# Kernel tuning notes

Hardware: AMD Instinct MI355X
Metric: run time of the kernel (lower is better)

The kernel has to match this reference:

```python
import jax, jax.numpy as jnp
from jax import lax
import numpy as np

K = 256   # kernel_size == hidden channels (Haar basis size)
S = 16    # stride
BN_EPS = 1e-5


def _haar_matrix_unnorm(n):
    if n == 2:
        return np.array([[1.0, 1.0], [1.0, -1.0]])
    prev = _haar_matrix_unnorm(n // 2)
    top = np.kron(prev, np.array([1.0, 1.0]))
    bot = np.kron(np.eye(n // 2), np.array([1.0, -1.0]))
    return np.concatenate((top, bot))


def haar_matrix(n):
    h = _haar_matrix_unnorm(n)
    return h / np.linalg.norm(h, axis=1, keepdims=True)


def setup_inputs() -> dict:
    key = jax.random.key(0)
    ks = jax.random.split(key, 8)
    B, T = 64, 32768
    haar = jnp.asarray(haar_matrix(K), dtype=jnp.float32)          # [K, K]
    x = jax.random.normal(ks[0], (B, 1, T), dtype=jnp.float32)
    return {
        "x": x,
        # BitwiseConv1d(1, K, K, stride=S, padding=K)
        "conv_w": haar[:, None, :],                                 # [K, 1, K] (OIH)
        "conv_b": 0.01 * jax.random.normal(ks[1], (K,), dtype=jnp.float32),
        "conv_gate": jax.random.uniform(ks[2], (K, 1, K), dtype=jnp.float32),
        "conv_scale": jnp.ones((K,), dtype=jnp.float32),            # adaptive per-out-channel scale
        # BatchNorm1d(K)
        "bn_gamma": jnp.ones((K,), dtype=jnp.float32),
        "bn_beta": jnp.zeros((K,), dtype=jnp.float32),
        # BitwiseConvTranspose1d(K, 1, K, stride=S)
        "ct_w": haar.T[:, None, :],                                 # [K(in), 1(out), K] (IOH, torch layout)
        "ct_b": 0.01 * jax.random.normal(ks[3], (1,), dtype=jnp.float32),
        "ct_gate": jax.random.uniform(ks[4], (K, 1, K), dtype=jnp.float32),
        "ct_scale": jnp.ones((1,), dtype=jnp.float32),
    }


def _forward(x, conv_w, conv_b, conv_gate, conv_scale, bn_gamma, bn_beta,
             ct_w, ct_b, ct_gate, ct_scale):
    T = x.shape[2]
    # --- BitwiseConv1d: gated weights (in_bin/weight_bin = identity) ---
    # gate binarization maps gate -> (gate + 1) / 2, multiplied into weights
    w = conv_w * (conv_gate + 1.0) * 0.5                            # [K,1,K]
    h = lax.conv_general_dilated(
        x, w, window_strides=(S,), padding=[(K, K)],
        dimension_numbers=("NCH", "OIH", "NCH"))                  # [B,K,L]
    h = conv_scale[None, :, None] * (h + conv_b[None, :, None])    # adaptive scaling
    # --- ReLU then BatchNorm1d (training-mode batch statistics) ---
    h = jax.nn.relu(h)
    mu = jnp.mean(h, axis=(0, 2), keepdims=True)
    var = jnp.mean((h - mu) ** 2, axis=(0, 2), keepdims=True)
    h = (h - mu) * lax.rsqrt(var + BN_EPS)
    h = h * bn_gamma[None, :, None] + bn_beta[None, :, None]
    # --- BitwiseConvTranspose1d: gated weights, expressed as dilated conv ---
    wt = ct_w * (ct_gate + 1.0) * 0.5                               # [K_in, 1, K]
    # torch IOH -> regular-conv OIH with kernel flipped
    wr = jnp.flip(jnp.transpose(wt, (1, 0, 2)), axis=-1)            # [1, K, K]
    y = lax.conv_general_dilated(
        h, wr, window_strides=(1,), padding=[(K - 1, K - 1)],
        lhs_dilation=(S,), dimension_numbers=("NCH", "OIH", "NCH"))
    y = ct_scale[None, :, None] * (y + ct_b[None, :, None])
    # crop: out[:, :, K : T + K]
    return y[:, :, K:T + K]


def reference(x, conv_w, conv_b, conv_gate, conv_scale, bn_gamma, bn_beta,
              ct_w, ct_b, ct_gate, ct_scale):
    return _forward(x, conv_w, conv_b, conv_gate, conv_scale, bn_gamma, bn_beta,
                    ct_w, ct_b, ct_gate, ct_scale)
```

## Files before the change

kernel.cpp:

```cpp
#include <hip/hip_runtime.h>
#include <hip/hip_bf16.h>

#define BB 64
#define TT 32768
#define KK 256
#define LL 2065
#define NLT 9
#define NPART (BB*NLT)
#define NJ 19
#define HBSTR 72
#define NPT3 8

typedef __attribute__((ext_vector_type(8))) short short8;
typedef __attribute__((ext_vector_type(4))) float f32x4;
typedef __attribute__((ext_vector_type(4))) int int4v;
typedef __attribute__((ext_vector_type(2))) unsigned int uint2v;

__device__ __forceinline__ unsigned short f2bf(float f) {
    unsigned u = __builtin_bit_cast(unsigned, f);
    unsigned r = (u + 0x7FFFu + ((u >> 16) & 1u)) >> 16;
    return (unsigned short)r;
}
__device__ __forceinline__ unsigned pkbf(float a, float b) {
    unsigned r;
    asm("v_cvt_pk_bf16_f32 %0, %1, %2" : "=v"(r) : "v"(a), "v"(b));
    return r;
}
__device__ __forceinline__ void gload_lds16(const void* g, void* l) {
    __builtin_amdgcn_global_load_lds(
        (const __attribute__((address_space(1))) unsigned int*)g,
        (__attribute__((address_space(3))) unsigned int*)l, 16, 0, 0);
}

__global__ void k0_w1f(const float* __restrict__ cw, const float* __restrict__ cgt,
                       unsigned short* __restrict__ W1f)
{
    int idx = blockIdx.x*256 + threadIdx.x;
    int lane = idx & 63, ntL = (idx>>6)&7, kk = (idx>>9)&7, half = idx>>12;
    int o = half*128 + ntL*16 + (lane&15);
    int kbase = kk*32 + ((lane>>4)<<3);
    short8 v;
    #pragma unroll
    for (int i = 0; i < 8; ++i) {
        int gi = o*KK + kbase + i;
        v[i] = (short)f2bf(cw[gi]*(cgt[gi]+1.0f)*0.5f);
    }
    *(short8*)(W1f + (size_t)idx*8) = v;
}

__global__ __launch_bounds__(256, 3)
void k1_conv(const float* __restrict__ x, const float* __restrict__ cs,
             const float* __restrict__ cb, const unsigned short* __restrict__ W1f,
             unsigned short* __restrict__ hout,
             float* __restrict__ psum, float* __restrict__ psq)
{
    __shared__ __align__(16) char smem[13056 + 32768];
    char* xwinb = smem;
    char* wbuf  = smem + 13056;
    unsigned short* hb = (unsigned short*)smem;
    float* redS = (float*)(smem + 36864);
    float* redQ = (float*)(smem + 36864 + 1024);

    const int tid   = threadIdx.x;
    const int q     = blockIdx.x & 3;
    const int ltile = blockIdx.x >> 2;
    const int b     = blockIdx.y;
    const int l0    = ltile * 256;
    const long pos0 = (long)l0*16 - 256;
    const int lane  = tid & 63;
    const int w     = tid >> 6;

    {
        #pragma unroll
        for (int it = 0; it < 8; ++it) {
            int ci = w*8 + it;
            int kk = ci >> 2, ntl = ci & 3;
            size_t so = (size_t)((((q>>1)*8 + kk)*8 + (q&1)*4 + ntl))*1024;
            gload_lds16((const char*)W1f + so + lane*16, wbuf + ci*1024);
        }
    }
    {
        const float* xs = x + (size_t)b*TT;
        for (int g = tid; g < 272; g += 256) {
            long base = pos0 + (long)g*16;
            unsigned uu[8];
            if (base >= 0 && base + 16 <= (long)TT) {
                const float4* xv = (const float4*)(xs + base);
                float4 a0 = xv[0], a1 = xv[1], a2 = xv[2], a3 = xv[3];
                uu[0] = pkbf(a0.x, a0.y); uu[1] = pkbf(a0.z, a0.w);
                uu[2] = pkbf(a1.x, a1.y); uu[3] = pkbf(a1.z, a1.w);
                uu[4] = pkbf(a2.x, a2.y); uu[5] = pkbf(a2.z, a2.w);
                uu[6] = pkbf(a3.x, a3.y); uu[7] = pkbf(a3.z, a3.w);
            } else {
                #pragma unroll
                for (int m = 0; m < 16; m += 2) {
                    long p = base + m;
                    float f0 = (p   >= 0 && p   < TT) ? xs[p]   : 0.0f;
                    float f1 = (p+1 >= 0 && p+1 < TT) ? xs[p+1] : 0.0f;
                    uu[m>>1] = pkbf(f0, f1);
                }
            }
            int4v w0 = { (int)uu[0], (int)uu[1], (int)uu[2], (int)uu[3] };
            int4v w1 = { (int)uu[4], (int)uu[5], (int)uu[6], (int)uu[7] };
            *(int4v*)(xwinb + 48*g)      = w0;
            *(int4v*)(xwinb + 48*g + 16) = w1;
        }
    }
    __syncthreads();

    f32x4 acc[4][4];
    #pragma unroll
    for (int mt = 0; mt < 4; ++mt)
        #pragma unroll
        for (int nt = 0; nt < 4; ++nt) acc[mt][nt] = (f32x4){0.f,0.f,0.f,0.f};

    const int gq = lane >> 4;
    const int Gt = 16*gq + 16*(gq>>1);
    const int abase = 48*((w<<6) + (lane & 15)) + Gt;

    #pragma unroll
    for (int kk = 0; kk < 8; ++kk) {
        short8 bfx[4], afw[4];
        #pragma unroll
        for (int nt = 0; nt < 4; ++nt)
            bfx[nt] = *(const short8*)(xwinb + abase + nt*768 + kk*96);
        #pragma unroll
        for (int mt = 0; mt < 4; ++mt)
            afw[mt] = *(const short8*)(wbuf + (kk*4 + mt)*1024 + lane*16);
        __builtin_amdgcn_s_setprio(1);
        #pragma unroll
        for (int mt = 0; mt < 4; ++mt)
            #pragma unroll
            for (int nt = 0; nt < 4; ++nt)
                acc[mt][nt] = __builtin_amdgcn_mfma_f32_16x16x32_bf16(afw[mt], bfx[nt], acc[mt][nt], 0, 0, 0);
        __builtin_amdgcn_s_setprio(0);
    }
    __syncthreads();

    const int c0 = q*64;
    const int g  = lane >> 4;
    const int li = lane & 15;
    #pragma unroll
    for (int mt = 0; mt < 4; ++mt) {
        int cq = c0 + mt*16 + g*4;
        f32x4 cs4 = *(const f32x4*)&cs[cq];
        f32x4 cb4 = *(const f32x4*)&cb[cq];
        f32x4 s4 = (f32x4){0.f,0.f,0.f,0.f};
        f32x4 q4 = (f32x4){0.f,0.f,0.f,0.f};
        #pragma unroll
        for (int nt = 0; nt < 4; ++nt) {
            int lloc = (w<<6) + nt*16 + li;
            f32x4 hv;
            #pragma unroll
            for (int rr = 0; rr < 4; ++rr)
                hv[rr] = fmaxf(cs4[rr]*(acc[mt][nt][rr] + cb4[rr]), 0.0f);
            uint2v pkv = { pkbf(hv[0], hv[1]), pkbf(hv[2], hv[3]) };
            *(uint2v*)(hb + lloc*HBSTR + mt*16 + g*4) = pkv;
            if (l0 + lloc < LL) { s4 += hv; q4 += hv*hv; }
        }
        #pragma unroll
        for (int d = 1; d < 16; d <<= 1) {
            #pragma unroll
            for (int rr = 0; rr < 4; ++rr) {
                s4[rr] += __shfl_xor(s4[rr], d);
                q4[rr] += __shfl_xor(q4[rr], d);
            }
        }
        if (li == 0) {
            *(f32x4*)&redS[((w*4 + mt)*4 + g)*4] = s4;
            *(f32x4*)&redQ[((w*4 + mt)*4 + g)*4] = q4;
        }
    }
    __syncthreads();

    {
        const int rsub = tid >> 3;
        const int cpos = tid & 7;
        #pragma unroll
        for (int it = 0; it < 8; ++it) {
            int row = it*32 + rsub;
            int l = l0 + row;
            if (l < LL) {
                int4v v = *(const int4v*)(hb + row*HBSTR + cpos*8);
                *(int4v*)(hout + (((size_t)(b*LL + l)) << 8) + q*64 + cpos*8) = v;
            }
        }
    }
    if (tid < 64) {
        int mt = tid >> 4, gg = (tid >> 2) & 3, rr = tid & 3;
        float s = 0.f, qq = 0.f;
        #pragma unroll
        for (int wv = 0; wv < 4; ++wv) {
            s  += redS[((wv*4 + mt)*4 + gg)*4 + rr];
            qq += redQ[((wv*4 + mt)*4 + gg)*4 + rr];
        }
        int c = c0 + tid;
        int slot = b*NLT + ltile;
        psum[c*NPART + slot] = s;
        psq [c*NPART + slot] = qq;
    }
}

__global__ __launch_bounds__(256)
void k2_bn(const float* __restrict__ psum, const float* __restrict__ psq,
           const float* __restrict__ bng, const float* __restrict__ bnb,
           const float* __restrict__ ctw, const float* __restrict__ ctg,
           const float* __restrict__ ctscale,
           float* __restrict__ W3s, float* __restrict__ SWS)
{
    __shared__ double rs[4], rq[4];
    __shared__ float s_a, s_bc;
    __shared__ float swl[256];
    const int c = blockIdx.x;
    const int tid = threadIdx.x;
    double s = 0.0, q = 0.0;
    for (int i = tid; i < NPART; i += 256) {
        s += (double)psum[c*NPART + i];
        q += (double)psq [c*NPART + i];
    }
    for (int off = 32; off > 0; off >>= 1) {
        s += __shfl_down(s, off);
        q += __shfl_down(q, off);
    }
    if ((tid & 63) == 0) { rs[tid >> 6] = s; rq[tid >> 6] = q; }
    __syncthreads();
    if (tid == 0) {
        double st = rs[0]+rs[1]+rs[2]+rs[3];
        double qt = rq[0]+rq[1]+rq[2]+rq[3];
        const double cnt = (double)BB * (double)LL;
        double mu = st / cnt;
        double var = qt / cnt - mu*mu;
        float rsig = (float)(1.0 / sqrt(var + 1e-5));
        float a = bng[c] * rsig;
        s_a = a;
        s_bc = bnb[c] - (float)mu * a;
    }
    __syncthreads();
    float a = s_a, bc = s_bc, scl = ctscale[0];
    int gi = c*KK + tid;
    float wt = ctw[gi] * (ctg[gi] + 1.0f) * 0.5f;
    W3s[tid*KK + c] = scl * a * wt;
    swl[tid] = wt * bc;
    __syncthreads();
    if (tid < 16) {
        float acc2 = 0.0f;
        #pragma unroll
        for (int d = 0; d < 16; ++d) acc2 += swl[d*16 + tid];
        SWS[c*16 + tid] = acc2;
    }
}

__global__ void k2b_const(const float* __restrict__ SWS, const float* __restrict__ ctb,
                          const float* __restrict__ ctscale, float* __restrict__ C2)
{
    int r = threadIdx.x;
    if (r < 16) {
        float s = 0.0f;
        for (int c = 0; c < 256; ++c) s += SWS[c*16 + r];
        C2[r] = ctscale[0] * (s + ctb[0]);
    }
}

__global__ void k2c_b2f(const float* __restrict__ W3s, unsigned short* __restrict__ B2f)
{
    int idx = blockIdx.x*256 + threadIdx.x;
    int lane = idx & 63;
    int ntG  = (idx>>6) & 3;
    int kk   = (idx>>8) & 7;
    int j    = idx>>11;
    int c    = kk*32 + ((lane>>4)<<3);
    int r    = lane & 15;
    int d    = ntG + 15 - j;
    short8 v;
    if (d >= 0 && d <= 15) {
        const float* wr = W3s + (size_t)(16*d + r)*KK + c;
        #pragma unroll
        for (int i = 0; i < 8; ++i) v[i] = (short)f2bf(wr[i]);
    } else {
        #pragma unroll
        for (int i = 0; i < 8; ++i) v[i] = 0;
    }
    *(short8*)(B2f + (size_t)idx*8) = v;
}

__global__ __launch_bounds__(512, 1)
void k3_synth(const unsigned short* __restrict__ h, const unsigned short* __restrict__ B2f,
              const float* __restrict__ C2, float* __restrict__ out)
{
    __shared__ __align__(16) char As[272*512];
    const int tid  = threadIdx.x;
    const int lane = tid & 63;
    const int w    = tid >> 6;
    const int b    = blockIdx.y;
    const int P0   = blockIdx.x * 64;

    const char* hbase = (const char*)h + (((size_t)(b*LL) + 4*P0 + 1) << 9);

    {
        const int rl = lane >> 5;
        #pragma unroll
        for (int i = 0; i < 17; ++i) {
            int r0  = w*34 + i*2;
            int row = r0 + rl;
            int chunk = (lane & 31) ^ ((row >> 2) & 7);
            gload_lds16(hbase + (size_t)row*512 + chunk*16, As + r0*512);
        }
    }
    __syncthreads();

    const int li = lane & 15;
    const int gq = lane >> 4;

    f32x4 acc[4][4];
    #pragma unroll
    for (int mt = 0; mt < 4; ++mt)
        #pragma unroll
        for (int nt = 0; nt < 4; ++nt) acc[mt][nt] = (f32x4){0.f,0.f,0.f,0.f};

    #pragma unroll 1
    for (int jj = 0; jj < 3; ++jj) {
        const int j = w + jj*8;
        if (j >= NJ) break;
        short8 bfA[4], bfB[4];
        #pragma unroll
        for (int nt = 0; nt < 4; ++nt)
            bfA[nt] = *(const short8*)(B2f + (((size_t)(j*8 + 0)*4 + nt)*64 + lane)*8);
        #pragma unroll
        for (int kk = 0; kk < 8; ++kk) {
            if (kk < 7) {
                #pragma unroll
                for (int nt = 0; nt < 4; ++nt)
                    bfB[nt] = *(const short8*)(B2f + (((size_t)(j*8 + kk+1)*4 + nt)*64 + lane)*8);
            }
            short8 af[4];
            #pragma unroll
            for (int mt = 0; mt < 4; ++mt) {
                int row = 64*mt + 4*li + j;
                int p = (kk*4 + gq) ^ ((row >> 2) & 7);
                af[mt] = *(const short8*)(As + row*512 + p*16);
            }
            __builtin_amdgcn_s_setprio(1);
            #pragma unroll
            for (int mt = 0; mt < 4; ++mt)
                #pragma unroll
                for (int nt = 0; nt < 4; ++nt)
                    acc[mt][nt] = __builtin_amdgcn_mfma_f32_16x16x32_bf16(af[mt], bfA[nt], acc[mt][nt], 0, 0, 0);
            __builtin_amdgcn_s_setprio(0);
            #pragma unroll
            for (int nt = 0; nt < 4; ++nt) bfA[nt] = bfB[nt];
        }
    }
    __syncthreads();

    float* red = (float*)As;
    #pragma unroll
    for (int mt = 0; mt < 4; ++mt)
        #pragma unroll
        for (int nt = 0; nt < 4; ++nt) {
            int u = nt*16 + li;
            #pragma unroll
            for (int rr = 0; rr < 4; ++rr) {
                int Pl = 16*mt + gq*4 + rr;
                red[w*4352 + Pl*68 + u] = acc[mt][nt][rr];
            }
        }
    __syncthreads();

    {
        float* ob = out + (size_t)b*TT + (size_t)P0*64;
        #pragma unroll
        for (int it = 0; it < 2; ++it) {
            int item = it*512 + tid;
            int P = item >> 4, uq = item & 15;
            f32x4 s = (f32x4){0.f,0.f,0.f,0.f};
            #pragma unroll
            for (int c = 0; c < 8; ++c)
                s += *(const f32x4*)&red[c*4352 + P*68 + uq*4];
            int ub = (uq & 3)*4;
            f32x4 c2v = { C2[ub], C2[ub+1], C2[ub+2], C2[ub+3] };
            *(f32x4*)&ob[P*64 + uq*4] = s + c2v;
        }
    }
}

extern "C" void kernel_launch(void* const* d_in, const int* in_sizes, int n_in,
                              void* d_out, int out_size, void* d_ws, size_t ws_size,
                              hipStream_t stream)
{
    const float* x       = (const float*)d_in[0];
    const float* cw      = (const float*)d_in[1];
    const float* cb      = (const float*)d_in[2];
    const float* cgt     = (const float*)d_in[3];
    const float* cs      = (const float*)d_in[4];
    const float* bng     = (const float*)d_in[5];
    const float* bnb     = (const float*)d_in[6];
    const float* ctw     = (const float*)d_in[7];
    const float* ctb     = (const float*)d_in[8];
    const float* ctg     = (const float*)d_in[9];
    const float* ctscale = (const float*)d_in[10];
    float* out = (float*)d_out;

    char* ws = (char*)d_ws;
    size_t off = 0;
    unsigned short* h    = (unsigned short*)(ws + off); off += (size_t)BB*LL*KK*2;
    float* psum          = (float*)(ws + off);          off += (size_t)KK*NPART*4;
    float* psq           = (float*)(ws + off);          off += (size_t)KK*NPART*4;
    unsigned short* W1f  = (unsigned short*)(ws + off); off += 65536*2;
    float* W3s           = (float*)(ws + off);          off += (size_t)KK*KK*4;
    float* SWS           = (float*)(ws + off);          off += (size_t)KK*16*4;
    float* C2            = (float*)(ws + off);          off += 64;
    unsigned short* B2f  = (unsigned short*)(ws + off); off += (size_t)NJ*8*4*64*8*2;

    k0_w1f  <<<32, 256, 0, stream>>>(cw, cgt, W1f);
    k1_conv <<<dim3(36, BB), 256, 0, stream>>>(x, cs, cb, W1f, h, psum, psq);
    k2_bn   <<<KK, 256, 0, stream>>>(psum, psq, bng, bnb, ctw, ctg, ctscale, W3s, SWS);
    k2b_const<<<1, 64, 0, stream>>>(SWS, ctb, ctscale, C2);
    k2c_b2f <<<152, 256, 0, stream>>>(W3s, B2f);
    k3_synth<<<dim3(NPT3, BB), 512, 0, stream>>>(h, B2f, C2, out);
}
```

Before: 83.52 us.

## Halve synthesis tile, fold conv scale into weights, shorten BN shuffle reduction

The synthesis kernel now processes 32 output frames per block instead of 64. That halves its LDS footprint and accumulator count, allows up to 4 blocks per CU, and doubles the grid. The conv scale is folded into the bf16 weights and a precomputed scaled bias, which removes a multiply per output in the conv epilogue. The per-channel stats reduction does fewer cross-lane shuffles and writes more partials to LDS, which are summed afterwards. Smaller tiles mean less reuse of each B2f fragment load, and folding the scale into the weights before bf16 rounding slightly changes numerics.

```diff
diff --git a/kernel.cpp b/kernel.cpp
--- a/kernel.cpp
+++ b/kernel.cpp
@@ -9,7 +9,7 @@
 #define NPART (BB*NLT)
 #define NJ 19
 #define HBSTR 72
-#define NPT3 8
+#define NPT3 16
 
 typedef __attribute__((ext_vector_type(8))) short short8;
 typedef __attribute__((ext_vector_type(4))) float f32x4;
@@ -33,24 +33,30 @@
 }
 
 __global__ void k0_w1f(const float* __restrict__ cw, const float* __restrict__ cgt,
-                       unsigned short* __restrict__ W1f)
+                       const float* __restrict__ cs, const float* __restrict__ cb,
+                       unsigned short* __restrict__ W1f, float* __restrict__ cbs)
 {
     int idx = blockIdx.x*256 + threadIdx.x;
     int lane = idx & 63, ntL = (idx>>6)&7, kk = (idx>>9)&7, half = idx>>12;
     int o = half*128 + ntL*16 + (lane&15);
+    float sc = cs[o];
     int kbase = kk*32 + ((lane>>4)<<3);
     short8 v;
     #pragma unroll
     for (int i = 0; i < 8; ++i) {
         int gi = o*KK + kbase + i;
-        v[i] = (short)f2bf(cw[gi]*(cgt[gi]+1.0f)*0.5f);
+        v[i] = (short)f2bf(sc * cw[gi]*(cgt[gi]+1.0f)*0.5f);
     }
     *(short8*)(W1f + (size_t)idx*8) = v;
+    if (blockIdx.x == 0) {
+        int c = threadIdx.x;
+        cbs[c] = cs[c]*cb[c];
+    }
 }
 
 __global__ __launch_bounds__(256, 3)
-void k1_conv(const float* __restrict__ x, const float* __restrict__ cs,
-             const float* __restrict__ cb, const unsigned short* __restrict__ W1f,
+void k1_conv(const float* __restrict__ x, const float* __restrict__ cbs,
+             const unsigned short* __restrict__ W1f,
              unsigned short* __restrict__ hout,
              float* __restrict__ psum, float* __restrict__ psq)
 {
@@ -59,7 +65,7 @@
     char* wbuf  = smem + 13056;
     unsigned short* hb = (unsigned short*)smem;
     float* redS = (float*)(smem + 36864);
-    float* redQ = (float*)(smem + 36864 + 1024);
+    float* redQ = (float*)(smem + 36864 + 4096);
 
     const int tid   = threadIdx.x;
     const int q     = blockIdx.x & 3;
@@ -143,8 +149,7 @@
     #pragma unroll
     for (int mt = 0; mt < 4; ++mt) {
         int cq = c0 + mt*16 + g*4;
-        f32x4 cs4 = *(const f32x4*)&cs[cq];
-        f32x4 cb4 = *(const f32x4*)&cb[cq];
+        f32x4 cbs4 = *(const f32x4*)&cbs[cq];
         f32x4 s4 = (f32x4){0.f,0.f,0.f,0.f};
         f32x4 q4 = (f32x4){0.f,0.f,0.f,0.f};
         #pragma unroll
@@ -153,22 +158,23 @@
             f32x4 hv;
             #pragma unroll
             for (int rr = 0; rr < 4; ++rr)
-                hv[rr] = fmaxf(cs4[rr]*(acc[mt][nt][rr] + cb4[rr]), 0.0f);
+                hv[rr] = fmaxf(acc[mt][nt][rr] + cbs4[rr], 0.0f);
             uint2v pkv = { pkbf(hv[0], hv[1]), pkbf(hv[2], hv[3]) };
             *(uint2v*)(hb + lloc*HBSTR + mt*16 + g*4) = pkv;
             if (l0 + lloc < LL) { s4 += hv; q4 += hv*hv; }
         }
         #pragma unroll
-        for (int d = 1; d < 16; d <<= 1) {
+        for (int d = 1; d < 4; d <<= 1) {
             #pragma unroll
             for (int rr = 0; rr < 4; ++rr) {
                 s4[rr] += __shfl_xor(s4[rr], d);
                 q4[rr] += __shfl_xor(q4[rr], d);
             }
         }
-        if (li == 0) {
-            *(f32x4*)&redS[((w*4 + mt)*4 + g)*4] = s4;
-            *(f32x4*)&redQ[((w*4 + mt)*4 + g)*4] = q4;
+        if ((li & 3) == 0) {
+            int slot = ((w*4 + mt)*4 + g)*4 + (li >> 2);
+            *(f32x4*)&redS[slot*4] = s4;
+            *(f32x4*)&redQ[slot*4] = q4;
         }
     }
     __syncthreads();
@@ -190,10 +196,13 @@
         int mt = tid >> 4, gg = (tid >> 2) & 3, rr = tid & 3;
         float s = 0.f, qq = 0.f;
         #pragma unroll
-        for (int wv = 0; wv < 4; ++wv) {
-            s  += redS[((wv*4 + mt)*4 + gg)*4 + rr];
-            qq += redQ[((wv*4 + mt)*4 + gg)*4 + rr];
-        }
+        for (int wv = 0; wv < 4; ++wv)
+            #pragma unroll
+            for (int l4 = 0; l4 < 4; ++l4) {
+                int slot = ((wv*4 + mt)*4 + gg)*4 + l4;
+                s  += redS[slot*4 + rr];
+                qq += redQ[slot*4 + rr];
+            }
         int c = c0 + tid;
         int slot = b*NLT + ltile;
         psum[c*NPART + slot] = s;
@@ -283,24 +292,24 @@
     *(short8*)(B2f + (size_t)idx*8) = v;
 }
 
-__global__ __launch_bounds__(512, 1)
+__global__ __launch_bounds__(512, 4)
 void k3_synth(const unsigned short* __restrict__ h, const unsigned short* __restrict__ B2f,
               const float* __restrict__ C2, float* __restrict__ out)
 {
-    __shared__ __align__(16) char As[272*512];
+    __shared__ __align__(16) char As[144*512];
     const int tid  = threadIdx.x;
     const int lane = tid & 63;
     const int w    = tid >> 6;
     const int b    = blockIdx.y;
-    const int P0   = blockIdx.x * 64;
+    const int P0   = blockIdx.x * 32;
 
     const char* hbase = (const char*)h + (((size_t)(b*LL) + 4*P0 + 1) << 9);
 
     {
         const int rl = lane >> 5;
         #pragma unroll
-        for (int i = 0; i < 17; ++i) {
-            int r0  = w*34 + i*2;
+        for (int i = 0; i < 9; ++i) {
+            int r0  = w*18 + i*2;
             int row = r0 + rl;
             int chunk = (lane & 31) ^ ((row >> 2) & 7);
             gload_lds16(hbase + (size_t)row*512 + chunk*16, As + r0*512);
@@ -311,9 +320,9 @@
     const int li = lane & 15;
     const int gq = lane >> 4;
 
-    f32x4 acc[4][4];
-    #pragma unroll
-    for (int mt = 0; mt < 4; ++mt)
+    f32x4 acc[2][4];
+    #pragma unroll
+    for (int mt = 0; mt < 2; ++mt)
         #pragma unroll
         for (int nt = 0; nt < 4; ++nt) acc[mt][nt] = (f32x4){0.f,0.f,0.f,0.f};
 
@@ -332,16 +341,16 @@
                 for (int nt = 0; nt < 4; ++nt)
                     bfB[nt] = *(const short8*)(B2f + (((size_t)(j*8 + kk+1)*4 + nt)*64 + lane)*8);
             }
-            short8 af[4];
-            #pragma unroll
-            for (int mt = 0; mt < 4; ++mt) {
+            short8 af[2];
+            #pragma unroll
+            for (int mt = 0; mt < 2; ++mt) {
                 int row = 64*mt + 4*li + j;
                 int p = (kk*4 + gq) ^ ((row >> 2) & 7);
                 af[mt] = *(const short8*)(As + row*512 + p*16);
             }
             __builtin_amdgcn_s_setprio(1);
             #pragma unroll
-            for (int mt = 0; mt < 4; ++mt)
+            for (int mt = 0; mt < 2; ++mt)
                 #pragma unroll
                 for (int nt = 0; nt < 4; ++nt)
                     acc[mt][nt] = __builtin_amdgcn_mfma_f32_16x16x32_bf16(af[mt], bfA[nt], acc[mt][nt], 0, 0, 0);
@@ -354,32 +363,28 @@
 
     float* red = (float*)As;
     #pragma unroll
-    for (int mt = 0; mt < 4; ++mt)
+    for (int mt = 0; mt < 2; ++mt)
         #pragma unroll
         for (int nt = 0; nt < 4; ++nt) {
             int u = nt*16 + li;
             #pragma unroll
             for (int rr = 0; rr < 4; ++rr) {
                 int Pl = 16*mt + gq*4 + rr;
-                red[w*4352 + Pl*68 + u] = acc[mt][nt][rr];
+                red[w*2176 + Pl*68 + u] = acc[mt][nt][rr];
             }
         }
     __syncthreads();
 
     {
+        int P = tid >> 4, uq = tid & 15;
+        f32x4 s = (f32x4){0.f,0.f,0.f,0.f};
+        #pragma unroll
+        for (int c = 0; c < 8; ++c)
+            s += *(const f32x4*)&red[c*2176 + P*68 + uq*4];
+        int ub = (uq & 3)*4;
+        f32x4 c2v = { C2[ub], C2[ub+1], C2[ub+2], C2[ub+3] };
         float* ob = out + (size_t)b*TT + (size_t)P0*64;
-        #pragma unroll
-        for (int it = 0; it < 2; ++it) {
-            int item = it*512 + tid;
-            int P = item >> 4, uq = item & 15;
-            f32x4 s = (f32x4){0.f,0.f,0.f,0.f};
-            #pragma unroll
-            for (int c = 0; c < 8; ++c)
-                s += *(const f32x4*)&red[c*4352 + P*68 + uq*4];
-            int ub = (uq & 3)*4;
-            f32x4 c2v = { C2[ub], C2[ub+1], C2[ub+2], C2[ub+3] };
-            *(f32x4*)&ob[P*64 + uq*4] = s + c2v;
-        }
+        *(f32x4*)&ob[P*64 + uq*4] = s + c2v;
     }
 }
 
@@ -409,10 +414,11 @@
     float* W3s           = (float*)(ws + off);          off += (size_t)KK*KK*4;
     float* SWS           = (float*)(ws + off);          off += (size_t)KK*16*4;
     float* C2            = (float*)(ws + off);          off += 64;
+    float* cbs           = (float*)(ws + off);          off += 1024;
     unsigned short* B2f  = (unsigned short*)(ws + off); off += (size_t)NJ*8*4*64*8*2;
 
-    k0_w1f  <<<32, 256, 0, stream>>>(cw, cgt, W1f);
-    k1_conv <<<dim3(36, BB), 256, 0, stream>>>(x, cs, cb, W1f, h, psum, psq);
+    k0_w1f  <<<32, 256, 0, stream>>>(cw, cgt, cs, cb, W1f, cbs);
+    k1_conv <<<dim3(36, BB), 256, 0, stream>>>(x, cbs, W1f, h, psum, psq);
     k2_bn   <<<KK, 256, 0, stream>>>(psum, psq, bng, bnb, ctw, ctg, ctscale, W3s, SWS);
     k2b_const<<<1, 64, 0, stream>>>(SWS, ctb, ctscale, C2);
     k2c_b2f <<<152, 256, 0, stream>>>(W3s, B2f);
```

Result: no change. 84.87 us (+1.6%).

## Split synthesis GEMM over K halves into two launches and skip zero weight tiles

Applied to the files above, without the earlier changes.

k3_synth now processes one half of the channel dimension per launch (z=0,1), using 256-thread blocks with half the LDS so two blocks fit per CU. The second launch reads back the first's partial output and adds the bias. Each wave gets a contiguous range of j values and skips MFMAs on B2f tiles that are known to be all zero. k2b_const's serial reduction becomes a 256-thread two-level reduction. The split adds an extra launch plus an output read-modify-write pass, and 19 j-values spread over 4 waves leaves them unevenly loaded.

```diff
diff --git a/kernel.cpp b/kernel.cpp
--- a/kernel.cpp
+++ b/kernel.cpp
@@ -9,7 +9,6 @@
 #define NPART (BB*NLT)
 #define NJ 19
 #define HBSTR 72
-#define NPT3 8
 
 typedef __attribute__((ext_vector_type(8))) short short8;
 typedef __attribute__((ext_vector_type(4))) float f32x4;
@@ -250,14 +249,23 @@
     }
 }
 
-__global__ void k2b_const(const float* __restrict__ SWS, const float* __restrict__ ctb,
-                          const float* __restrict__ ctscale, float* __restrict__ C2)
-{
-    int r = threadIdx.x;
-    if (r < 16) {
-        float s = 0.0f;
-        for (int c = 0; c < 256; ++c) s += SWS[c*16 + r];
-        C2[r] = ctscale[0] * (s + ctb[0]);
+__global__ __launch_bounds__(256)
+void k2b_const(const float* __restrict__ SWS, const float* __restrict__ ctb,
+               const float* __restrict__ ctscale, float* __restrict__ C2)
+{
+    __shared__ float accb[16][17];
+    int tid = threadIdx.x;
+    int r = tid & 15, cc = tid >> 4;
+    float s = 0.0f;
+    #pragma unroll
+    for (int i = 0; i < 16; ++i) s += SWS[(cc*16 + i)*16 + r];
+    accb[cc][r] = s;
+    __syncthreads();
+    if (tid < 16) {
+        float t = 0.0f;
+        #pragma unroll
+        for (int i = 0; i < 16; ++i) t += accb[i][tid];
+        C2[tid] = ctscale[0] * (t + ctb[0]);
     }
 }
 
@@ -283,11 +291,11 @@
     *(short8*)(B2f + (size_t)idx*8) = v;
 }
 
-__global__ __launch_bounds__(512, 1)
+__global__ __launch_bounds__(256, 2)
 void k3_synth(const unsigned short* __restrict__ h, const unsigned short* __restrict__ B2f,
-              const float* __restrict__ C2, float* __restrict__ out)
-{
-    __shared__ __align__(16) char As[272*512];
+              const float* __restrict__ C2, float* __restrict__ out, int z)
+{
+    __shared__ __align__(16) char As[272*256];
     const int tid  = threadIdx.x;
     const int lane = tid & 63;
     const int w    = tid >> 6;
@@ -296,15 +304,12 @@
 
     const char* hbase = (const char*)h + (((size_t)(b*LL) + 4*P0 + 1) << 9);
 
-    {
-        const int rl = lane >> 5;
-        #pragma unroll
-        for (int i = 0; i < 17; ++i) {
-            int r0  = w*34 + i*2;
-            int row = r0 + rl;
-            int chunk = (lane & 31) ^ ((row >> 2) & 7);
-            gload_lds16(hbase + (size_t)row*512 + chunk*16, As + r0*512);
-        }
+    #pragma unroll
+    for (int i = 0; i < 17; ++i) {
+        int item = i*256 + tid;
+        int row = item >> 4, ck = item & 15;
+        int sck = ck ^ ((row >> 2) & 15);
+        gload_lds16(hbase + (size_t)row*512 + z*256 + sck*16, As + item*16);
     }
     __syncthreads();
 
@@ -317,37 +322,35 @@
         #pragma unroll
         for (int nt = 0; nt < 4; ++nt) acc[mt][nt] = (f32x4){0.f,0.f,0.f,0.f};
 
+    const int j0 = w*5;
+    const int j1 = (w < 3) ? w*5 + 5 : NJ;
     #pragma unroll 1
-    for (int jj = 0; jj < 3; ++jj) {
-        const int j = w + jj*8;
-        if (j >= NJ) break;
-        short8 bfA[4], bfB[4];
-        #pragma unroll
-        for (int nt = 0; nt < 4; ++nt)
-            bfA[nt] = *(const short8*)(B2f + (((size_t)(j*8 + 0)*4 + nt)*64 + lane)*8);
-        #pragma unroll
-        for (int kk = 0; kk < 8; ++kk) {
-            if (kk < 7) {
-                #pragma unroll
-                for (int nt = 0; nt < 4; ++nt)
-                    bfB[nt] = *(const short8*)(B2f + (((size_t)(j*8 + kk+1)*4 + nt)*64 + lane)*8);
-            }
+    for (int j = j0; j < j1; ++j) {
+        const int ntlo = (j > 15) ? j - 15 : 0;
+        const int nthi = (j < 3) ? j : 3;
+        #pragma unroll
+        for (int kk = 0; kk < 4; ++kk) {
+            const int kkg = z*4 + kk;
+            short8 bfr[4];
+            #pragma unroll
+            for (int nt = 0; nt < 4; ++nt)
+                if (nt >= ntlo && nt <= nthi)
+                    bfr[nt] = *(const short8*)(B2f + (((size_t)(j*8 + kkg)*4 + nt)*64 + lane)*8);
             short8 af[4];
             #pragma unroll
             for (int mt = 0; mt < 4; ++mt) {
                 int row = 64*mt + 4*li + j;
-                int p = (kk*4 + gq) ^ ((row >> 2) & 7);
-                af[mt] = *(const short8*)(As + row*512 + p*16);
+                int ckp = (kk*4 + gq) ^ ((row >> 2) & 15);
+                af[mt] = *(const short8*)(As + row*256 + ckp*16);
             }
             __builtin_amdgcn_s_setprio(1);
             #pragma unroll
             for (int mt = 0; mt < 4; ++mt)
                 #pragma unroll
                 for (int nt = 0; nt < 4; ++nt)
-                    acc[mt][nt] = __builtin_amdgcn_mfma_f32_16x16x32_bf16(af[mt], bfA[nt], acc[mt][nt], 0, 0, 0);
+                    if (nt >= ntlo && nt <= nthi)
+                        acc[mt][nt] = __builtin_amdgcn_mfma_f32_16x16x32_bf16(af[mt], bfr[nt], acc[mt][nt], 0, 0, 0);
             __builtin_amdgcn_s_setprio(0);
-            #pragma unroll
-            for (int nt = 0; nt < 4; ++nt) bfA[nt] = bfB[nt];
         }
     }
     __syncthreads();
@@ -369,16 +372,21 @@
     {
         float* ob = out + (size_t)b*TT + (size_t)P0*64;
         #pragma unroll
-        for (int it = 0; it < 2; ++it) {
-            int item = it*512 + tid;
+        for (int i = 0; i < 4; ++i) {
+            int item = i*256 + tid;
             int P = item >> 4, uq = item & 15;
             f32x4 s = (f32x4){0.f,0.f,0.f,0.f};
             #pragma unroll
-            for (int c = 0; c < 8; ++c)
+            for (int c = 0; c < 4; ++c)
                 s += *(const f32x4*)&red[c*4352 + P*68 + uq*4];
-            int ub = (uq & 3)*4;
-            f32x4 c2v = { C2[ub], C2[ub+1], C2[ub+2], C2[ub+3] };
-            *(f32x4*)&ob[P*64 + uq*4] = s + c2v;
+            if (z == 0) {
+                *(f32x4*)&ob[P*64 + uq*4] = s;
+            } else {
+                int ub = (uq & 3)*4;
+                f32x4 c2v = { C2[ub], C2[ub+1], C2[ub+2], C2[ub+3] };
+                f32x4 prev = *(const f32x4*)&ob[P*64 + uq*4];
+                *(f32x4*)&ob[P*64 + uq*4] = prev + s + c2v;
+            }
         }
     }
 }
@@ -414,7 +422,8 @@
     k0_w1f  <<<32, 256, 0, stream>>>(cw, cgt, W1f);
     k1_conv <<<dim3(36, BB), 256, 0, stream>>>(x, cs, cb, W1f, h, psum, psq);
     k2_bn   <<<KK, 256, 0, stream>>>(psum, psq, bng, bnb, ctw, ctg, ctscale, W3s, SWS);
-    k2b_const<<<1, 64, 0, stream>>>(SWS, ctb, ctscale, C2);
+    k2b_const<<<1, 256, 0, stream>>>(SWS, ctb, ctscale, C2);
     k2c_b2f <<<152, 256, 0, stream>>>(W3s, B2f);
-    k3_synth<<<dim3(NPT3, BB), 512, 0, stream>>>(h, B2f, C2, out);
-}
+    k3_synth<<<dim3(8, BB), 256, 0, stream>>>(h, B2f, C2, out, 0);
+    k3_synth<<<dim3(8, BB), 256, 0, stream>>>(h, B2f, C2, out, 1);
+}
```

After: 92.97 us. +11.3%, slower.
